# Optimization experiments

Hardware: AMD Instinct MI355X
Metric: run time of the kernel (lower is better)

The kernel has to match this reference:

```python
import jax, jax.numpy as jnp
import numpy as np
from itertools import permutations

B, L, H, A, E, R, BS = 4, 1024, 768, 12, 32, 97, 64
P = E * (E - 1)  # ordered entity pairs per sample
HTS = np.array(list(permutations(range(E), 2)), dtype=np.int32)  # [P,2]


def setup_inputs() -> dict:
    key = jax.random.key(0)
    ks = jax.random.split(key, 8)
    return {
        "hidden_state": jax.random.normal(ks[0], (B, L, H), jnp.float32),
        "attention": jax.random.uniform(ks[1], (B, A, L, L), jnp.float32),
        "attention_mask": jnp.ones((B, L), jnp.float32),
        "head": jax.random.randint(ks[2], (B, E), 0, L, jnp.int32),
        "tail": jax.random.randint(ks[3], (B, E), 0, L, jnp.int32),
        # params (stored [in, out])
        "Wh": jax.random.normal(ks[4], (2 * H, H), jnp.float32) * 0.02,
        "bh": jnp.zeros((H,), jnp.float32),
        "Wt": jax.random.normal(ks[5], (2 * H, H), jnp.float32) * 0.02,
        "bt": jnp.zeros((H,), jnp.float32),
        "Wc": jax.random.normal(ks[6], (H * BS, R), jnp.float32) * 0.01,
        "bc": jnp.zeros((R,), jnp.float32),
    }


def reference(hidden_state, attention, attention_mask, head, tail, Wh, bh, Wt, bt, Wc, bc):
    attn = attention.mean(axis=1)  # [B,L,L]
    hts0 = jnp.asarray(HTS[:, 0])
    hts1 = jnp.asarray(HTS[:, 1])

    def per_sample(hid, at, hd, tl, am):
        ent_feat = (hid[hd] + hid[tl]) * 0.5   # [E,H]
        ent_attn = (at[hd] + at[tl]) * 0.5     # [E,L]
        head_f = ent_feat[hts0]                # [P,H]
        tail_f = ent_feat[hts1]                # [P,H]
        ht_attn = ent_attn[hts0] * ent_attn[hts1] * am  # [P,L]
        ht_attn = ht_attn / (ht_attn.sum(-1, keepdims=True) + 1e-20)
        ht_info = ht_attn @ hid                # [P,H]
        return (jnp.concatenate([head_f, ht_info], -1),
                jnp.concatenate([tail_f, ht_info], -1))

    all_h, all_t = jax.vmap(per_sample)(hidden_state, attn, head, tail, attention_mask)
    all_h = all_h.reshape(-1, 2 * H)  # [B*P, 2H]
    all_t = all_t.reshape(-1, 2 * H)
    h = jnp.tanh(all_h @ Wh + bh)     # [N,H]
    t = jnp.tanh(all_t @ Wt + bt)
    N = h.shape[0]
    # GroupLinear: block-diagonal outer product then linear
    outer = (h.reshape(N, H // BS, BS, 1) * t.reshape(N, H // BS, 1, BS)).reshape(N, H * BS)
    logits = outer @ Wc + bc          # [N,R]
    return logits
```

## Files before the change

### kernel.cpp

```cpp
#include <hip/hip_runtime.h>
#include <cstdint>
#include <cstddef>

#define BB 4
#define LL 1024
#define HH 768
#define AA 12
#define EE 32
#define PP 992
#define PPAD 1024
#define NROW (BB*PPAD)
#define NN (BB*PP)
#define RR 97
#define RP 112
#define GS2 16

typedef __attribute__((ext_vector_type(8))) _Float16 half8;
typedef __attribute__((ext_vector_type(4))) _Float16 half4v;
typedef __attribute__((ext_vector_type(2))) _Float16 half2v;
typedef __attribute__((ext_vector_type(4))) float floatx4;

union H8u { half8 v8; half2v v2[4]; };

#define WAITVM(N) asm volatile("s_waitcnt vmcnt(" #N ")" ::: "memory")

__device__ __forceinline__ void gl_lds16(const void* g, void* l) {
    __builtin_amdgcn_global_load_lds(
        (const __attribute__((address_space(1))) unsigned int*)g,
        (__attribute__((address_space(3))) unsigned int*)l, 16, 0, 0);
}

__device__ __forceinline__ void barrier_raw() {
    asm volatile("" ::: "memory");
    __builtin_amdgcn_s_barrier();
    __builtin_amdgcn_sched_barrier(0);
    asm volatile("" ::: "memory");
}

__device__ __forceinline__ int xswz96(int bid) {
    return (bid & 7) * 96 + (bid >> 3);
}

__device__ __forceinline__ void pair_decode(int p, int& i0, int& i1) {
    i0 = p / 31;
    int r = p - i0 * 31;
    i1 = r + (r >= i0 ? 1 : 0);
}

__device__ __forceinline__ float fast_tanh(float x) {
    float ax = fabsf(x);
    float t = __builtin_amdgcn_exp2f(ax * -2.885390082f);
    float r = (1.f - t) * __builtin_amdgcn_rcpf(1.f + t);
    return copysignf(r, x);
}

__global__ __launch_bounds__(256) void k_stage0(
        const float* __restrict__ hid, const float* __restrict__ att,
        const int* __restrict__ head, const int* __restrict__ tail,
        const float* __restrict__ Wh, const float* __restrict__ Wt,
        const float* __restrict__ Wc,
        _Float16* __restrict__ hidb, _Float16* __restrict__ Whf,
        _Float16* __restrict__ Wtf, _Float16* __restrict__ W1hf,
        _Float16* __restrict__ W1tf, _Float16* __restrict__ Wcp,
        float* __restrict__ ent_attn) {
    __shared__ float ldw[32][101];
    int bid = blockIdx.x, tid = threadIdx.x;
    if (bid < 1536) {
        int ksg = bid;
        int w = tid >> 6, lane = tid & 63;
        const float* src = Wc + (size_t)ksg * 32 * RR;
        #pragma unroll
        for (int rr = 0; rr < 8; ++rr) {
            int row = w * 8 + rr;
            ldw[row][lane] = src[(size_t)row * RR + lane];
            if (lane < 33) ldw[row][64 + lane] = src[(size_t)row * RR + 64 + lane];
        }
        __syncthreads();
        #pragma unroll
        for (int j = 0; j < 2; ++j) {
            int f = tid + j * 256;
            int rt = f >> 6, lf = f & 63;
            int c = rt * 16 + (lf & 15);
            int kb = (lf >> 4) * 8;
            _Float16 v[8];
            #pragma unroll
            for (int e = 0; e < 8; ++e)
                v[e] = (c < RR) ? (_Float16)ldw[kb + e][c] : (_Float16)0.f;
            *(half8*)(Wcp + ((size_t)ksg * 512 + f) * 8) = *(const half8*)v;
        }
    } else if (bid < 2112) {
        int which = (bid < 1824) ? 0 : 1;
        const float* src = (which ? Wt : Wh) + (size_t)HH * HH;
        _Float16* dst = which ? Wtf : Whf;
        int idx = (bid - (which ? 1824 : 1536)) * 256 + tid;
        int lane = idx & 63, f = idx >> 6;
        int ct = f % 48, ks = f / 48;
        int c = ct * 16 + (lane & 15);
        int kb = ks * 32 + (lane >> 4) * 8;
        _Float16 v[8];
        #pragma unroll
        for (int e = 0; e < 8; ++e)
            v[e] = (_Float16)src[(size_t)(kb + e) * HH + c];
        *(half8*)(dst + (size_t)idx * 8) = *(const half8*)v;
    } else if (bid < 3648) {
        int idx = (bid - 2112) * 256 + tid;
        const float* s = hid + (size_t)idx * 8;
        float4 a = *(const float4*)s;
        float4 b = *(const float4*)(s + 4);
        half8 v = { (_Float16)a.x, (_Float16)a.y, (_Float16)a.z, (_Float16)a.w,
                    (_Float16)b.x, (_Float16)b.y, (_Float16)b.z, (_Float16)b.w };
        *(half8*)(hidb + (size_t)idx * 8) = v;
    } else if (bid < 4160) {
        int q = bid - 3648;
        int be = q >> 2, qt = q & 3;
        int b = be >> 5;
        int hd = head[be], tl = tail[be];
        const float* abase = att + (size_t)b * AA * LL * LL;
        int ll = qt * 256 + tid;
        float s = 0.f;
        #pragma unroll
        for (int a = 0; a < AA; ++a) {
            const float* ar = abase + (size_t)a * LL * LL;
            s += ar[(size_t)hd * LL + ll] + ar[(size_t)tl * LL + ll];
        }
        ent_attn[(size_t)be * LL + ll] = s * (0.5f / AA);
    } else {
        int which = (bid < 4448) ? 0 : 1;
        const float* src = which ? Wt : Wh;
        _Float16* dst = which ? W1tf : W1hf;
        int idx = (bid - (which ? 4448 : 4160)) * 256 + tid;
        int lane = idx & 63, f = idx >> 6;
        int ct = f % 48, ks = f / 48;
        int c = ct * 16 + (lane & 15);
        int kb = ks * 32 + (lane >> 4) * 8;
        _Float16 v[8];
        #pragma unroll
        for (int e = 0; e < 8; ++e)
            v[e] = (_Float16)src[(size_t)(kb + e) * HH + c];
        *(half8*)(dst + (size_t)idx * 8) = *(const half8*)v;
    }
}

__global__ __launch_bounds__(256) void k_stage1(
        const float* __restrict__ ent_attn, const float* __restrict__ am,
        const int* __restrict__ head, const int* __restrict__ tail,
        const _Float16* __restrict__ hidb,
        const _Float16* __restrict__ W1hf, const _Float16* __restrict__ W1tf,
        const float* __restrict__ bh, const float* __restrict__ bt,
        _Float16* __restrict__ pairw, float* __restrict__ Fht) {
    int tid = threadIdx.x;
    if (blockIdx.x < 1024) {
        int lane = tid & 63, w = tid >> 6;
        int prow = blockIdx.x * 4 + w;
        int b = prow >> 10, p = prow & 1023;
        _Float16* dst = pairw + (size_t)prow * LL;
        if (p >= PP) {
            #pragma unroll
            for (int c = 0; c < 4; ++c) {
                half4v z = {};
                *(half4v*)(dst + c * 256 + lane * 4) = z;
            }
            return;
        }
        int i0, i1; pair_decode(p, i0, i1);
        const float* e0  = ent_attn + ((size_t)b * EE + i0) * LL;
        const float* e1  = ent_attn + ((size_t)b * EE + i1) * LL;
        const float* amr = am + (size_t)b * LL;
        float wv[16];
        float s = 0.f;
        #pragma unroll
        for (int c = 0; c < 4; ++c) {
            int o = c * 256 + lane * 4;
            float4 a = *(const float4*)(e0 + o);
            float4 d = *(const float4*)(e1 + o);
            float4 m = *(const float4*)(amr + o);
            wv[c*4+0] = a.x * d.x * m.x; wv[c*4+1] = a.y * d.y * m.y;
            wv[c*4+2] = a.z * d.z * m.z; wv[c*4+3] = a.w * d.w * m.w;
            s += wv[c*4+0] + wv[c*4+1] + wv[c*4+2] + wv[c*4+3];
        }
        #pragma unroll
        for (int off = 32; off > 0; off >>= 1) s += __shfl_down(s, off, 64);
        float tot = __shfl(s, 0, 64);
        float inv = 1.0f / (tot + 1e-20f);
        #pragma unroll
        for (int c = 0; c < 4; ++c) {
            half4v o4 = { (_Float16)(wv[c*4+0] * inv), (_Float16)(wv[c*4+1] * inv),
                          (_Float16)(wv[c*4+2] * inv), (_Float16)(wv[c*4+3] * inv) };
            *(half4v*)(dst + c * 256 + lane * 4) = o4;
        }
    } else {
        int q = blockIdx.x - 1024;
        int ct = q % 12, b = (q / 12) % BB, mat = q / 48;
        const _Float16* Wf = mat ? W1tf : W1hf;
        const float* bias = mat ? bt : bh;
        int lane = tid & 63, w = tid >> 6;
        int row = (w & 1) * 16 + (lane & 15);
        int k8 = (lane >> 4) * 8;
        int hd = head[b * EE + row], tl = tail[b * EE + row];
        const _Float16* Ah = hidb + ((size_t)b * LL + hd) * HH + k8;
        const _Float16* At = hidb + ((size_t)b * LL + tl) * HH + k8;
        int ctG0 = ct * 4 + (w >> 1) * 2;
        const half8* B0 = (const half8*)Wf + (size_t)ctG0 * 64 + lane;
        floatx4 acc[2] = {};
        half2v hlf = { (_Float16)0.5f, (_Float16)0.5f };
        for (int ks = 0; ks < 24; ++ks) {
            H8u a_, b_, av;
            a_.v8 = *(const half8*)(Ah + ks * 32);
            b_.v8 = *(const half8*)(At + ks * 32);
            #pragma unroll
            for (int qq = 0; qq < 4; ++qq) av.v2[qq] = (a_.v2[qq] + b_.v2[qq]) * hlf;
            const half8* Bk = B0 + (size_t)ks * 48 * 64;
            acc[0] = __builtin_amdgcn_mfma_f32_16x16x32_f16(av.v8, Bk[0], acc[0], 0, 0, 0);
            acc[1] = __builtin_amdgcn_mfma_f32_16x16x32_f16(av.v8, Bk[64], acc[1], 0, 0, 0);
        }
        int rb = lane & 15, u = lane >> 4;
        #pragma unroll
        for (int cc = 0; cc < 2; ++cc) {
            int c = (ctG0 + cc) * 16 + rb;
            float bi = bias[c];
            float* dst = Fht + (((size_t)mat * BB + b) * EE + (w & 1) * 16 + u * 4) * HH + c;
            #pragma unroll
            for (int qq = 0; qq < 4; ++qq)
                dst[(size_t)qq * HH] = acc[cc][qq] + bi;
        }
    }
}

__global__ __launch_bounds__(128) void k_vgemm(
        const _Float16* __restrict__ hidb,
        const _Float16* __restrict__ Whf, const _Float16* __restrict__ Wtf,
        _Float16* __restrict__ Vhf, _Float16* __restrict__ Vtf) {
    int bid = xswz96(blockIdx.x);
    int cb = bid >> 6, mI = bid & 63;
    int ct0 = cb * 4;
    __shared__ __align__(16) _Float16 Bs[4][4096];
    int tid = threadIdx.x, lane = tid & 63, wid = tid >> 6;
    int r0 = wid * 32 + (lane & 15);
    int kg8 = (lane >> 4) * 8;

    const _Float16* A0 = hidb + (size_t)(mI * 64 + r0) * HH + kg8;
    const _Float16* A1 = A0 + 16 * HH;
    const char* WhB = (const char*)Whf + (size_t)ct0 * 1024;
    const char* WtB = (const char*)Wtf + (size_t)ct0 * 1024;
    char* LB = (char*)&Bs[0][0];
    int lo = wid * 2048 + lane * 16;
    int ld = wid * 2048;

    #pragma unroll
    for (int j = 0; j < 2; ++j) {
        gl_lds16(WhB + j * 1024 + lo, LB + j * 1024 + ld);
        gl_lds16(WtB + j * 1024 + lo, LB + 4096 + j * 1024 + ld);
    }
    half8 a0c = *(const half8*)A0;
    half8 a1c = *(const half8*)A1;
    {
        const char* hs = WhB + 49152;
        const char* ts = WtB + 49152;
        #pragma unroll
        for (int j = 0; j < 2; ++j) {
            gl_lds16(hs + j * 1024 + lo, LB + 8192 + j * 1024 + ld);
            gl_lds16(ts + j * 1024 + lo, LB + 8192 + 4096 + j * 1024 + ld);
        }
    }
    floatx4 aH[2][4] = {}, aT[2][4] = {};
    half8 a0n = a0c, a1n = a1c;
    for (int ks = 0; ks < 24; ++ks) {
        int buf = ks & 3;
        if (ks < 23) {
            a0n = *(const half8*)(A0 + (ks + 1) * 32);
            a1n = *(const half8*)(A1 + (ks + 1) * 32);
        }
        if (ks < 22) {
            const char* hs = WhB + (size_t)(ks + 2) * 49152;
            const char* ts = WtB + (size_t)(ks + 2) * 49152;
            char* lb = LB + ((ks + 2) & 3) * 8192;
            #pragma unroll
            for (int j = 0; j < 2; ++j) {
                gl_lds16(hs + j * 1024 + lo, lb + j * 1024 + ld);
                gl_lds16(ts + j * 1024 + lo, lb + 4096 + j * 1024 + ld);
            }
            WAITVM(12);
        } else if (ks == 22) { WAITVM(8); } else { WAITVM(2); }
        barrier_raw();
        const half8* bp = (const half8*)(LB + buf * 8192) + lane;
        __builtin_amdgcn_s_setprio(1);
        #pragma unroll
        for (int ct = 0; ct < 4; ++ct) {
            half8 bvh = bp[ct * 64];
            half8 bvt = bp[256 + ct * 64];
            aH[0][ct] = __builtin_amdgcn_mfma_f32_16x16x32_f16(a0c, bvh, aH[0][ct], 0, 0, 0);
            aH[1][ct] = __builtin_amdgcn_mfma_f32_16x16x32_f16(a1c, bvh, aH[1][ct], 0, 0, 0);
            aT[0][ct] = __builtin_amdgcn_mfma_f32_16x16x32_f16(a0c, bvt, aT[0][ct], 0, 0, 0);
            aT[1][ct] = __builtin_amdgcn_mfma_f32_16x16x32_f16(a1c, bvt, aT[1][ct], 0, 0, 0);
        }
        __builtin_amdgcn_s_setprio(0);
        a0c = a0n; a1c = a1n;
    }
    int b = mI >> 4;
    int kspB = (mI & 15) * 2 + wid;
    int u = lane >> 4, rb = lane & 15;
    int estart = (u & 1) * 4;
    size_t bofs = (size_t)b * 786432;
    #pragma unroll
    for (int rs = 0; rs < 2; ++rs) {
        int laneL = (rs * 2 + (u >> 1)) * 16 + rb;
        #pragma unroll
        for (int ct = 0; ct < 4; ++ct) {
            size_t base = bofs + ((size_t)(kspB * 48 + ct0 + ct) * 64 + laneL) * 8 + estart;
            half4v hv = { (_Float16)aH[rs][ct][0], (_Float16)aH[rs][ct][1],
                          (_Float16)aH[rs][ct][2], (_Float16)aH[rs][ct][3] };
            half4v tv = { (_Float16)aT[rs][ct][0], (_Float16)aT[rs][ct][1],
                          (_Float16)aT[rs][ct][2], (_Float16)aT[rs][ct][3] };
            *(half4v*)(Vhf + base) = hv;
            *(half4v*)(Vtf + base) = tv;
        }
    }
}

__global__ __launch_bounds__(128) void k_proj_mfma(
        const _Float16* __restrict__ pairw,
        const _Float16* __restrict__ Vhf, const _Float16* __restrict__ Vtf,
        const float* __restrict__ Fht,
        _Float16* __restrict__ hb, _Float16* __restrict__ tb) {
    int bid = xswz96(blockIdx.x);
    int bc = bid >> 4, mI = bid & 15;
    int b = bc / 12, cb = bc - b * 12;
    int ct0 = cb * 4;
    __shared__ __align__(16) _Float16 Bs[4][4096];
    int tid = threadIdx.x, lane = tid & 63, wid = tid >> 6;
    int r0 = wid * 32 + (lane & 15);
    int kg8 = (lane >> 4) * 8;

    const _Float16* A0 = pairw + (size_t)(b * PPAD + mI * 64 + r0) * LL + kg8;
    const _Float16* A1 = A0 + 16 * LL;
    const char* VhB = (const char*)(Vhf + (size_t)b * 786432) + (size_t)ct0 * 1024;
    const char* VtB = (const char*)(Vtf + (size_t)b * 786432) + (size_t)ct0 * 1024;
    char* LB = (char*)&Bs[0][0];
    int lo = wid * 2048 + lane * 16;
    int ld = wid * 2048;

    #pragma unroll
    for (int j = 0; j < 2; ++j) {
        gl_lds16(VhB + j * 1024 + lo, LB + j * 1024 + ld);
        gl_lds16(VtB + j * 1024 + lo, LB + 4096 + j * 1024 + ld);
    }
    half8 a0c = *(const half8*)A0;
    half8 a1c = *(const half8*)A1;
    {
        const char* hs = VhB + 49152;
        const char* ts = VtB + 49152;
        #pragma unroll
        for (int j = 0; j < 2; ++j) {
            gl_lds16(hs + j * 1024 + lo, LB + 8192 + j * 1024 + ld);
            gl_lds16(ts + j * 1024 + lo, LB + 8192 + 4096 + j * 1024 + ld);
        }
    }
    floatx4 aH[2][4] = {}, aT4[2][4] = {};
    half8 a0n = a0c, a1n = a1c;
    for (int ks = 0; ks < 32; ++ks) {
        int buf = ks & 3;
        if (ks < 31) {
            a0n = *(const half8*)(A0 + (ks + 1) * 32);
            a1n = *(const half8*)(A1 + (ks + 1) * 32);
        }
        if (ks < 30) {
            const char* hs = VhB + (size_t)(ks + 2) * 49152;
            const char* ts = VtB + (size_t)(ks + 2) * 49152;
            char* lb = LB + ((ks + 2) & 3) * 8192;
            #pragma unroll
            for (int j = 0; j < 2; ++j) {
                gl_lds16(hs + j * 1024 + lo, lb + j * 1024 + ld);
                gl_lds16(ts + j * 1024 + lo, lb + 4096 + j * 1024 + ld);
            }
            WAITVM(12);
        } else if (ks == 30) { WAITVM(8); } else { WAITVM(2); }
        barrier_raw();
        const half8* bp = (const half8*)(LB + buf * 8192) + lane;
        __builtin_amdgcn_s_setprio(1);
        #pragma unroll
        for (int ct = 0; ct < 4; ++ct) {
            half8 bvh = bp[ct * 64];
            half8 bvt = bp[256 + ct * 64];
            aH[0][ct]  = __builtin_amdgcn_mfma_f32_16x16x32_f16(a0c, bvh, aH[0][ct], 0, 0, 0);
            aH[1][ct]  = __builtin_amdgcn_mfma_f32_16x16x32_f16(a1c, bvh, aH[1][ct], 0, 0, 0);
            aT4[0][ct] = __builtin_amdgcn_mfma_f32_16x16x32_f16(a0c, bvt, aT4[0][ct], 0, 0, 0);
            aT4[1][ct] = __builtin_amdgcn_mfma_f32_16x16x32_f16(a1c, bvt, aT4[1][ct], 0, 0, 0);
        }
        __builtin_amdgcn_s_setprio(0);
        a0c = a0n; a1c = a1n;
    }
    const float* FhB = Fht + (size_t)b * EE * HH;
    const float* FtB = Fht + (size_t)(BB + b) * EE * HH;
    int u = lane >> 4, rb = lane & 15;
    #pragma unroll
    for (int rs = 0; rs < 2; ++rs) {
        int pb = mI * 64 + wid * 32 + rs * 16 + u * 4;
        int i0a[4], i1a[4];
        #pragma unroll
        for (int q = 0; q < 4; ++q) {
            int p = pb + q;
            if (p < PP) pair_decode(p, i0a[q], i1a[q]);
            else { i0a[q] = -1; i1a[q] = -1; }
        }
        #pragma unroll
        for (int ct = 0; ct < 4; ++ct) {
            int c = (ct0 + ct) * 16 + rb;
            #pragma unroll
            for (int q = 0; q < 4; ++q) {
                size_t row = (size_t)b * PPAD + pb + q;
                _Float16 hv = (_Float16)0.f, tv = (_Float16)0.f;
                if (i0a[q] >= 0) {
                    hv = (_Float16)fast_tanh(aH[rs][ct][q]  + FhB[(size_t)i0a[q] * HH + c]);
                    tv = (_Float16)fast_tanh(aT4[rs][ct][q] + FtB[(size_t)i1a[q] * HH + c]);
                }
                hb[row * HH + c] = hv;
                tb[row * HH + c] = tv;
            }
        }
    }
}

__global__ __launch_bounds__(256) void k_logits_mfma(
        const _Float16* __restrict__ hb, const _Float16* __restrict__ tb,
        const _Float16* __restrict__ Wcp, _Float16* __restrict__ part) {
    int bid = blockIdx.x;
    int gs = (bid & 7) * 2 + ((bid >> 3) & 1);
    int nb = bid >> 4;
    int n0 = nb * 128;
    int hcol0 = gs * 48;
    int g0 = (3 * gs) >> 2;
    int tcol0 = g0 * 64;
    __shared__ __align__(16) _Float16 hT[6][128][8];
    __shared__ __align__(16) _Float16 tT[16][128][8];
    __shared__ __align__(16) _Float16 Bs[4][4096];
    int tid = threadIdx.x, lane = tid & 63, wid = tid >> 6;

    #pragma unroll
    for (int it = 0; it < 3; ++it) {
        int idx = tid + it * 256;
        int ch = idx >> 7, row = idx & 127;
        *(half8*)&hT[ch][row][0] =
            *(const half8*)(hb + (size_t)(n0 + row) * HH + hcol0 + ch * 8);
    }
    int nch = (HH - tcol0) >> 3;
    #pragma unroll
    for (int it = 0; it < 8; ++it) {
        int idx = tid + it * 256;
        int ch = idx >> 7, row = idx & 127;
        if (ch < nch)
            *(half8*)&tT[ch][row][0] =
                *(const half8*)(tb + (size_t)(n0 + row) * HH + tcol0 + ch * 8);
    }
    __syncthreads();

    const char* WcB = (const char*)Wcp + (size_t)gs * 96 * 8192;
    char* LB = (char*)&Bs[0][0];
    int lo = wid * 2048 + lane * 16;
    int ld = wid * 2048;
    #pragma unroll
    for (int s = 0; s < 2; ++s) {
        const char* sp = WcB + (size_t)s * 8192;
        char* lb = LB + s * 8192;
        gl_lds16(sp + lo, lb + ld);
        gl_lds16(sp + 1024 + lo, lb + 1024 + ld);
    }
    int r0 = wid * 32 + (lane & 15);
    int kgrp = lane >> 4;
    floatx4 acc[2][7] = {};

    for (int ks = 0; ks < 96; ++ks) {
        int buf = ks & 3;
        int ksg = gs * 96 + ks;
        int g = ksg >> 7;
        int kin = ksg & 127;
        int i = kin >> 1, jh = kin & 1;
        int hloc = g * 64 + i - hcol0;
        int chT = ((g * 64 + jh * 32 - tcol0) >> 3) + kgrp;
        _Float16 h0 = hT[hloc >> 3][r0][hloc & 7];
        _Float16 h1 = hT[hloc >> 3][r0 + 16][hloc & 7];
        H8u t0u, t1u, a0, a1;
        t0u.v8 = *(const half8*)&tT[chT][r0][0];
        t1u.v8 = *(const half8*)&tT[chT][r0 + 16][0];
        half2v h02 = { h0, h0 }, h12 = { h1, h1 };
        #pragma unroll
        for (int q = 0; q < 4; ++q) {
            a0.v2[q] = h02 * t0u.v2[q];
            a1.v2[q] = h12 * t1u.v2[q];
        }
        if (ks < 94) {
            const char* sp = WcB + (size_t)(ks + 2) * 8192;
            char* lb = LB + ((ks + 2) & 3) * 8192;
            gl_lds16(sp + lo, lb + ld);
            gl_lds16(sp + 1024 + lo, lb + 1024 + ld);
            WAITVM(4);
        } else if (ks == 94) { WAITVM(2); } else { WAITVM(0); }
        barrier_raw();
        const half8* bp = (const half8*)(LB + buf * 8192) + lane;
        __builtin_amdgcn_s_setprio(1);
        #pragma unroll
        for (int rt = 0; rt < 7; ++rt) {
            half8 bv = bp[rt * 64];
            acc[0][rt] = __builtin_amdgcn_mfma_f32_16x16x32_f16(a0.v8, bv, acc[0][rt], 0, 0, 0);
            acc[1][rt] = __builtin_amdgcn_mfma_f32_16x16x32_f16(a1.v8, bv, acc[1][rt], 0, 0, 0);
        }
        __builtin_amdgcn_s_setprio(0);
    }
    int rb = lane & 15, u = lane >> 4;
    #pragma unroll
    for (int rs = 0; rs < 2; ++rs) {
        int nbase = n0 + wid * 32 + rs * 16 + u * 4;
        #pragma unroll
        for (int rt = 0; rt < 7; ++rt)
            #pragma unroll
            for (int q = 0; q < 4; ++q)
                part[((size_t)gs * NROW + nbase + q) * RP + rt * 16 + rb] =
                    (_Float16)acc[rs][rt][q];
    }
}

__global__ __launch_bounds__(256) void k_reduce(
        const _Float16* __restrict__ part, const float* __restrict__ bc,
        float* __restrict__ out) {
    int idx = blockIdx.x * 256 + threadIdx.x;
    if (idx >= NN * RR) return;
    int n = idx / RR;
    int r = idx - n * RR;
    int b = n / PP, p = n - b * PP;
    size_t rowp = (size_t)b * PPAD + p;
    float s = bc[r];
    #pragma unroll
    for (int g = 0; g < GS2; ++g)
        s += (float)part[((size_t)g * NROW + rowp) * RP + r];
    out[idx] = s;
}

extern "C" void kernel_launch(void* const* d_in, const int* in_sizes, int n_in,
                              void* d_out, int out_size, void* d_ws, size_t ws_size,
                              hipStream_t stream) {
    const float* hid  = (const float*)d_in[0];
    const float* att  = (const float*)d_in[1];
    const float* am   = (const float*)d_in[2];
    const int*   head = (const int*)d_in[3];
    const int*   tail = (const int*)d_in[4];
    const float* Wh   = (const float*)d_in[5];
    const float* bh   = (const float*)d_in[6];
    const float* Wt   = (const float*)d_in[7];
    const float* bt   = (const float*)d_in[8];
    const float* Wc   = (const float*)d_in[9];
    const float* bc   = (const float*)d_in[10];
    float* out = (float*)d_out;

    char* w = (char*)d_ws;
    _Float16* Wcp = (_Float16*)w;  w += (size_t)1536 * 512 * 8 * 2;
    _Float16* Vhf = (_Float16*)w;  w += (size_t)BB * 786432 * 2;
    _Float16* Vtf = (_Float16*)w;  w += (size_t)BB * 786432 * 2;
    _Float16* hbv = (_Float16*)w;  w += (size_t)NROW * HH * 2;
    _Float16* tbv = (_Float16*)w;  w += (size_t)NROW * HH * 2;
    float* Fht      = (float*)w;   w += (size_t)2 * BB * EE * HH * 4;
    float* ent_attn = (float*)w;   w += (size_t)BB * EE * LL * 4;
    char* alias = w;
    _Float16* hidb  = (_Float16*)alias;
    _Float16* Whf   = (_Float16*)(alias + 6291456);
    _Float16* Wtf   = (_Float16*)(alias + 6291456 + 1179648);
    _Float16* pairw = (_Float16*)(alias + 6291456 + 2 * 1179648);
    _Float16* W1hf  = (_Float16*)(alias + 6291456 + 2 * 1179648 + 8388608);
    _Float16* W1tf  = (_Float16*)(alias + 6291456 + 3 * 1179648 + 8388608);
    _Float16* part  = (_Float16*)alias;

    k_stage0<<<4736, 256, 0, stream>>>(hid, att, head, tail, Wh, Wt, Wc,
                                       hidb, Whf, Wtf, W1hf, W1tf, Wcp, ent_attn);
    k_stage1<<<1120, 256, 0, stream>>>(ent_attn, am, head, tail, hidb,
                                       W1hf, W1tf, bh, bt, pairw, Fht);
    k_vgemm<<<768, 128, 0, stream>>>(hidb, Whf, Wtf, Vhf, Vtf);
    k_proj_mfma<<<768, 128, 0, stream>>>(pairw, Vhf, Vtf, Fht, hbv, tbv);
    k_logits_mfma<<<512, 256, 0, stream>>>(hbv, tbv, Wcp, part);
    k_reduce<<<1504, 256, 0, stream>>>(part, bc, out);
}
```

Measured before the change: 132.6 us.

## Fuse V-GEMM into stage1 launch and retile GEMMs to three column tiles

Merges the separate V-projection GEMM kernel into the stage1 kernel as extra blocks, so the pair-weight, entity-projection and V-GEMM work run in one launch. This removes a kernel boundary and lets independent work overlap. Both the V-GEMM and the projection GEMM now use 3 column tiles per block instead of 4, giving 1024 blocks instead of 768, with each wave loading only its own (h or t) weight slice into LDS. The pair-weight and Fht branches are reshaped to 128-thread blocks. The cost is less reuse per block, more blocks overall, and a mixed-workload kernel whose blocks are imbalanced.

```diff
diff --git a/kernel.cpp b/kernel.cpp
--- a/kernel.cpp
+++ b/kernel.cpp
@@ -35,10 +35,6 @@
     __builtin_amdgcn_s_barrier();
     __builtin_amdgcn_sched_barrier(0);
     asm volatile("" ::: "memory");
-}
-
-__device__ __forceinline__ int xswz96(int bid) {
-    return (bid & 7) * 96 + (bid >> 3);
 }
 
 __device__ __forceinline__ void pair_decode(int p, int& i0, int& i1) {
@@ -141,17 +137,92 @@
     }
 }
 
-__global__ __launch_bounds__(256) void k_stage1(
+__global__ __launch_bounds__(128) void k_mid(
         const float* __restrict__ ent_attn, const float* __restrict__ am,
         const int* __restrict__ head, const int* __restrict__ tail,
         const _Float16* __restrict__ hidb,
+        const _Float16* __restrict__ Whf, const _Float16* __restrict__ Wtf,
         const _Float16* __restrict__ W1hf, const _Float16* __restrict__ W1tf,
         const float* __restrict__ bh, const float* __restrict__ bt,
-        _Float16* __restrict__ pairw, float* __restrict__ Fht) {
-    int tid = threadIdx.x;
-    if (blockIdx.x < 1024) {
-        int lane = tid & 63, w = tid >> 6;
-        int prow = blockIdx.x * 4 + w;
+        _Float16* __restrict__ pairw, float* __restrict__ Fht,
+        _Float16* __restrict__ Vhf, _Float16* __restrict__ Vtf) {
+    __shared__ __align__(16) _Float16 Bs[4][3072];
+    int bid0 = blockIdx.x, tid = threadIdx.x;
+    int lane = tid & 63, wid = tid >> 6;
+    if (bid0 < 1024) {
+        int sw = (bid0 & 7) * 128 + (bid0 >> 3);
+        int cb = sw >> 6, mI = sw & 63;
+        int ct0 = cb * 3;
+        int r0 = wid * 32 + (lane & 15);
+        int kg8 = (lane >> 4) * 8;
+        const _Float16* A0 = hidb + (size_t)(mI * 64 + r0) * HH + kg8;
+        const _Float16* A1 = A0 + 16 * HH;
+        const char* mySrc = (wid ? (const char*)Wtf : (const char*)Whf)
+                            + (size_t)ct0 * 1024;
+        int myOff = wid ? 3072 : 0;
+        char* LB = (char*)&Bs[0][0];
+
+        #pragma unroll
+        for (int j = 0; j < 3; ++j)
+            gl_lds16(mySrc + j * 1024 + lane * 16, LB + myOff + j * 1024);
+        half8 a0c = *(const half8*)A0;
+        half8 a1c = *(const half8*)A1;
+        #pragma unroll
+        for (int j = 0; j < 3; ++j)
+            gl_lds16(mySrc + 49152 + j * 1024 + lane * 16, LB + 6144 + myOff + j * 1024);
+
+        floatx4 aH[2][3] = {}, aT[2][3] = {};
+        half8 a0n = a0c, a1n = a1c;
+        for (int ks = 0; ks < 24; ++ks) {
+            int buf = ks & 3;
+            if (ks < 23) {
+                a0n = *(const half8*)(A0 + (ks + 1) * 32);
+                a1n = *(const half8*)(A1 + (ks + 1) * 32);
+            }
+            if (ks < 22) {
+                const char* sp = mySrc + (size_t)(ks + 2) * 49152;
+                char* lb = LB + ((ks + 2) & 3) * 6144 + myOff;
+                #pragma unroll
+                for (int j = 0; j < 3; ++j)
+                    gl_lds16(sp + j * 1024 + lane * 16, lb + j * 1024);
+                WAITVM(10);
+            } else if (ks == 22) { WAITVM(6); } else { WAITVM(0); }
+            barrier_raw();
+            const half8* bp = (const half8*)(LB + buf * 6144) + lane;
+            __builtin_amdgcn_s_setprio(1);
+            #pragma unroll
+            for (int ct = 0; ct < 3; ++ct) {
+                half8 bvh = bp[ct * 64];
+                half8 bvt = bp[192 + ct * 64];
+                aH[0][ct] = __builtin_amdgcn_mfma_f32_16x16x32_f16(a0c, bvh, aH[0][ct], 0, 0, 0);
+                aH[1][ct] = __builtin_amdgcn_mfma_f32_16x16x32_f16(a1c, bvh, aH[1][ct], 0, 0, 0);
+                aT[0][ct] = __builtin_amdgcn_mfma_f32_16x16x32_f16(a0c, bvt, aT[0][ct], 0, 0, 0);
+                aT[1][ct] = __builtin_amdgcn_mfma_f32_16x16x32_f16(a1c, bvt, aT[1][ct], 0, 0, 0);
+            }
+            __builtin_amdgcn_s_setprio(0);
+            a0c = a0n; a1c = a1n;
+        }
+        int b = mI >> 4;
+        int kspB = (mI & 15) * 2 + wid;
+        int u = lane >> 4, rb = lane & 15;
+        int estart = (u & 1) * 4;
+        size_t bofs = (size_t)b * 786432;
+        #pragma unroll
+        for (int rs = 0; rs < 2; ++rs) {
+            int laneL = (rs * 2 + (u >> 1)) * 16 + rb;
+            #pragma unroll
+            for (int ct = 0; ct < 3; ++ct) {
+                size_t base = bofs + ((size_t)(kspB * 48 + ct0 + ct) * 64 + laneL) * 8 + estart;
+                half4v hv = { (_Float16)aH[rs][ct][0], (_Float16)aH[rs][ct][1],
+                              (_Float16)aH[rs][ct][2], (_Float16)aH[rs][ct][3] };
+                half4v tv = { (_Float16)aT[rs][ct][0], (_Float16)aT[rs][ct][1],
+                              (_Float16)aT[rs][ct][2], (_Float16)aT[rs][ct][3] };
+                *(half4v*)(Vhf + base) = hv;
+                *(half4v*)(Vtf + base) = tv;
+            }
+        }
+    } else if (bid0 < 3072) {
+        int prow = (bid0 - 1024) * 2 + wid;
         int b = prow >> 10, p = prow & 1023;
         _Float16* dst = pairw + (size_t)prow * LL;
         if (p >= PP) {
@@ -189,17 +260,18 @@
             *(half4v*)(dst + c * 256 + lane * 4) = o4;
         }
     } else {
-        int q = blockIdx.x - 1024;
-        int ct = q % 12, b = (q / 12) % BB, mat = q / 48;
+        int q = bid0 - 3072;
+        int chalf = q & 1;
+        int rest = q >> 1;
+        int ct = rest % 12, b = (rest / 12) & 3, mat = rest / 48;
         const _Float16* Wf = mat ? W1tf : W1hf;
         const float* bias = mat ? bt : bh;
-        int lane = tid & 63, w = tid >> 6;
-        int row = (w & 1) * 16 + (lane & 15);
+        int row = wid * 16 + (lane & 15);
         int k8 = (lane >> 4) * 8;
         int hd = head[b * EE + row], tl = tail[b * EE + row];
         const _Float16* Ah = hidb + ((size_t)b * LL + hd) * HH + k8;
         const _Float16* At = hidb + ((size_t)b * LL + tl) * HH + k8;
-        int ctG0 = ct * 4 + (w >> 1) * 2;
+        int ctG0 = ct * 4 + chalf * 2;
         const half8* B0 = (const half8*)Wf + (size_t)ctG0 * 64 + lane;
         floatx4 acc[2] = {};
         half2v hlf = { (_Float16)0.5f, (_Float16)0.5f };
@@ -218,101 +290,10 @@
         for (int cc = 0; cc < 2; ++cc) {
             int c = (ctG0 + cc) * 16 + rb;
             float bi = bias[c];
-            float* dst = Fht + (((size_t)mat * BB + b) * EE + (w & 1) * 16 + u * 4) * HH + c;
+            float* dst = Fht + (((size_t)mat * BB + b) * EE + wid * 16 + u * 4) * HH + c;
             #pragma unroll
             for (int qq = 0; qq < 4; ++qq)
                 dst[(size_t)qq * HH] = acc[cc][qq] + bi;
-        }
-    }
-}
-
-__global__ __launch_bounds__(128) void k_vgemm(
-        const _Float16* __restrict__ hidb,
-        const _Float16* __restrict__ Whf, const _Float16* __restrict__ Wtf,
-        _Float16* __restrict__ Vhf, _Float16* __restrict__ Vtf) {
-    int bid = xswz96(blockIdx.x);
-    int cb = bid >> 6, mI = bid & 63;
-    int ct0 = cb * 4;
-    __shared__ __align__(16) _Float16 Bs[4][4096];
-    int tid = threadIdx.x, lane = tid & 63, wid = tid >> 6;
-    int r0 = wid * 32 + (lane & 15);
-    int kg8 = (lane >> 4) * 8;
-
-    const _Float16* A0 = hidb + (size_t)(mI * 64 + r0) * HH + kg8;
-    const _Float16* A1 = A0 + 16 * HH;
-    const char* WhB = (const char*)Whf + (size_t)ct0 * 1024;
-    const char* WtB = (const char*)Wtf + (size_t)ct0 * 1024;
-    char* LB = (char*)&Bs[0][0];
-    int lo = wid * 2048 + lane * 16;
-    int ld = wid * 2048;
-
-    #pragma unroll
-    for (int j = 0; j < 2; ++j) {
-        gl_lds16(WhB + j * 1024 + lo, LB + j * 1024 + ld);
-        gl_lds16(WtB + j * 1024 + lo, LB + 4096 + j * 1024 + ld);
-    }
-    half8 a0c = *(const half8*)A0;
-    half8 a1c = *(const half8*)A1;
-    {
-        const char* hs = WhB + 49152;
-        const char* ts = WtB + 49152;
-        #pragma unroll
-        for (int j = 0; j < 2; ++j) {
-            gl_lds16(hs + j * 1024 + lo, LB + 8192 + j * 1024 + ld);
-            gl_lds16(ts + j * 1024 + lo, LB + 8192 + 4096 + j * 1024 + ld);
-        }
-    }
-    floatx4 aH[2][4] = {}, aT[2][4] = {};
-    half8 a0n = a0c, a1n = a1c;
-    for (int ks = 0; ks < 24; ++ks) {
-        int buf = ks & 3;
-        if (ks < 23) {
-            a0n = *(const half8*)(A0 + (ks + 1) * 32);
-            a1n = *(const half8*)(A1 + (ks + 1) * 32);
-        }
-        if (ks < 22) {
-            const char* hs = WhB + (size_t)(ks + 2) * 49152;
-            const char* ts = WtB + (size_t)(ks + 2) * 49152;
-            char* lb = LB + ((ks + 2) & 3) * 8192;
-            #pragma unroll
-            for (int j = 0; j < 2; ++j) {
-                gl_lds16(hs + j * 1024 + lo, lb + j * 1024 + ld);
-                gl_lds16(ts + j * 1024 + lo, lb + 4096 + j * 1024 + ld);
-            }
-            WAITVM(12);
-        } else if (ks == 22) { WAITVM(8); } else { WAITVM(2); }
-        barrier_raw();
-        const half8* bp = (const half8*)(LB + buf * 8192) + lane;
-        __builtin_amdgcn_s_setprio(1);
-        #pragma unroll
-        for (int ct = 0; ct < 4; ++ct) {
-            half8 bvh = bp[ct * 64];
-            half8 bvt = bp[256 + ct * 64];
-            aH[0][ct] = __builtin_amdgcn_mfma_f32_16x16x32_f16(a0c, bvh, aH[0][ct], 0, 0, 0);
-            aH[1][ct] = __builtin_amdgcn_mfma_f32_16x16x32_f16(a1c, bvh, aH[1][ct], 0, 0, 0);
-            aT[0][ct] = __builtin_amdgcn_mfma_f32_16x16x32_f16(a0c, bvt, aT[0][ct], 0, 0, 0);
-            aT[1][ct] = __builtin_amdgcn_mfma_f32_16x16x32_f16(a1c, bvt, aT[1][ct], 0, 0, 0);
-        }
-        __builtin_amdgcn_s_setprio(0);
-        a0c = a0n; a1c = a1n;
-    }
-    int b = mI >> 4;
-    int kspB = (mI & 15) * 2 + wid;
-    int u = lane >> 4, rb = lane & 15;
-    int estart = (u & 1) * 4;
-    size_t bofs = (size_t)b * 786432;
-    #pragma unroll
-    for (int rs = 0; rs < 2; ++rs) {
-        int laneL = (rs * 2 + (u >> 1)) * 16 + rb;
-        #pragma unroll
-        for (int ct = 0; ct < 4; ++ct) {
-            size_t base = bofs + ((size_t)(kspB * 48 + ct0 + ct) * 64 + laneL) * 8 + estart;
-            half4v hv = { (_Float16)aH[rs][ct][0], (_Float16)aH[rs][ct][1],
-                          (_Float16)aH[rs][ct][2], (_Float16)aH[rs][ct][3] };
-            half4v tv = { (_Float16)aT[rs][ct][0], (_Float16)aT[rs][ct][1],
-                          (_Float16)aT[rs][ct][2], (_Float16)aT[rs][ct][3] };
-            *(half4v*)(Vhf + base) = hv;
-            *(half4v*)(Vtf + base) = tv;
         }
     }
 }
@@ -322,40 +303,33 @@
         const _Float16* __restrict__ Vhf, const _Float16* __restrict__ Vtf,
         const float* __restrict__ Fht,
         _Float16* __restrict__ hb, _Float16* __restrict__ tb) {
-    int bid = xswz96(blockIdx.x);
-    int bc = bid >> 4, mI = bid & 15;
-    int b = bc / 12, cb = bc - b * 12;
-    int ct0 = cb * 4;
-    __shared__ __align__(16) _Float16 Bs[4][4096];
+    int sw = (blockIdx.x & 7) * 128 + (blockIdx.x >> 3);
+    int mI = sw & 15;
+    int bc = sw >> 4;
+    int b = bc >> 4, cb = bc & 15;
+    int ct0 = cb * 3;
+    __shared__ __align__(16) _Float16 Bs[4][3072];
     int tid = threadIdx.x, lane = tid & 63, wid = tid >> 6;
     int r0 = wid * 32 + (lane & 15);
     int kg8 = (lane >> 4) * 8;
 
     const _Float16* A0 = pairw + (size_t)(b * PPAD + mI * 64 + r0) * LL + kg8;
     const _Float16* A1 = A0 + 16 * LL;
-    const char* VhB = (const char*)(Vhf + (size_t)b * 786432) + (size_t)ct0 * 1024;
-    const char* VtB = (const char*)(Vtf + (size_t)b * 786432) + (size_t)ct0 * 1024;
+    const char* mySrc = ((wid ? (const char*)Vtf : (const char*)Vhf)
+                         + (size_t)b * 1572864) + (size_t)ct0 * 1024;
+    int myOff = wid ? 3072 : 0;
     char* LB = (char*)&Bs[0][0];
-    int lo = wid * 2048 + lane * 16;
-    int ld = wid * 2048;
-
-    #pragma unroll
-    for (int j = 0; j < 2; ++j) {
-        gl_lds16(VhB + j * 1024 + lo, LB + j * 1024 + ld);
-        gl_lds16(VtB + j * 1024 + lo, LB + 4096 + j * 1024 + ld);
-    }
+
+    #pragma unroll
+    for (int j = 0; j < 3; ++j)
+        gl_lds16(mySrc + j * 1024 + lane * 16, LB + myOff + j * 1024);
     half8 a0c = *(const half8*)A0;
     half8 a1c = *(const half8*)A1;
-    {
-        const char* hs = VhB + 49152;
-        const char* ts = VtB + 49152;
-        #pragma unroll
-        for (int j = 0; j < 2; ++j) {
-            gl_lds16(hs + j * 1024 + lo, LB + 8192 + j * 1024 + ld);
-            gl_lds16(ts + j * 1024 + lo, LB + 8192 + 4096 + j * 1024 + ld);
-        }
-    }
-    floatx4 aH[2][4] = {}, aT4[2][4] = {};
+    #pragma unroll
+    for (int j = 0; j < 3; ++j)
+        gl_lds16(mySrc + 49152 + j * 1024 + lane * 16, LB + 6144 + myOff + j * 1024);
+
+    floatx4 aH[2][3] = {}, aT4[2][3] = {};
     half8 a0n = a0c, a1n = a1c;
     for (int ks = 0; ks < 32; ++ks) {
         int buf = ks & 3;
@@ -364,23 +338,20 @@
             a1n = *(const half8*)(A1 + (ks + 1) * 32);
         }
         if (ks < 30) {
-            const char* hs = VhB + (size_t)(ks + 2) * 49152;
-            const char* ts = VtB + (size_t)(ks + 2) * 49152;
-            char* lb = LB + ((ks + 2) & 3) * 8192;
-            #pragma unroll
-            for (int j = 0; j < 2; ++j) {
-                gl_lds16(hs + j * 1024 + lo, lb + j * 1024 + ld);
-                gl_lds16(ts + j * 1024 + lo, lb + 4096 + j * 1024 + ld);
-            }
-            WAITVM(12);
-        } else if (ks == 30) { WAITVM(8); } else { WAITVM(2); }
+            const char* sp = mySrc + (size_t)(ks + 2) * 49152;
+            char* lb = LB + ((ks + 2) & 3) * 6144 + myOff;
+            #pragma unroll
+            for (int j = 0; j < 3; ++j)
+                gl_lds16(sp + j * 1024 + lane * 16, lb + j * 1024);
+            WAITVM(10);
+        } else if (ks == 30) { WAITVM(6); } else { WAITVM(0); }
         barrier_raw();
-        const half8* bp = (const half8*)(LB + buf * 8192) + lane;
+        const half8* bp = (const half8*)(LB + buf * 6144) + lane;
         __builtin_amdgcn_s_setprio(1);
         #pragma unroll
-        for (int ct = 0; ct < 4; ++ct) {
+        for (int ct = 0; ct < 3; ++ct) {
             half8 bvh = bp[ct * 64];
-            half8 bvt = bp[256 + ct * 64];
+            half8 bvt = bp[192 + ct * 64];
             aH[0][ct]  = __builtin_amdgcn_mfma_f32_16x16x32_f16(a0c, bvh, aH[0][ct], 0, 0, 0);
             aH[1][ct]  = __builtin_amdgcn_mfma_f32_16x16x32_f16(a1c, bvh, aH[1][ct], 0, 0, 0);
             aT4[0][ct] = __builtin_amdgcn_mfma_f32_16x16x32_f16(a0c, bvt, aT4[0][ct], 0, 0, 0);
@@ -403,7 +374,7 @@
             else { i0a[q] = -1; i1a[q] = -1; }
         }
         #pragma unroll
-        for (int ct = 0; ct < 4; ++ct) {
+        for (int ct = 0; ct < 3; ++ct) {
             int c = (ct0 + ct) * 16 + rb;
             #pragma unroll
             for (int q = 0; q < 4; ++q) {
@@ -569,10 +540,10 @@
 
     k_stage0<<<4736, 256, 0, stream>>>(hid, att, head, tail, Wh, Wt, Wc,
                                        hidb, Whf, Wtf, W1hf, W1tf, Wcp, ent_attn);
-    k_stage1<<<1120, 256, 0, stream>>>(ent_attn, am, head, tail, hidb,
-                                       W1hf, W1tf, bh, bt, pairw, Fht);
-    k_vgemm<<<768, 128, 0, stream>>>(hidb, Whf, Wtf, Vhf, Vtf);
-    k_proj_mfma<<<768, 128, 0, stream>>>(pairw, Vhf, Vtf, Fht, hbv, tbv);
+    k_mid<<<3264, 128, 0, stream>>>(ent_attn, am, head, tail, hidb,
+                                    Whf, Wtf, W1hf, W1tf, bh, bt,
+                                    pairw, Fht, Vhf, Vtf);
+    k_proj_mfma<<<1024, 128, 0, stream>>>(pairw, Vhf, Vtf, Fht, hbv, tbv);
     k_logits_mfma<<<512, 256, 0, stream>>>(hbv, tbv, Wcp, part);
     k_reduce<<<1504, 256, 0, stream>>>(part, bc, out);
 }
```

After: 140.7 us. 1.06x slower.
